# Kernel tuning notes

Hardware: AMD Instinct MI355X
Metric: run time of the kernel (lower is better)

Reference implementation:

```python
import jax, jax.numpy as jnp
import numpy as np
import math

H, NH, LAT = 2048, 16, 512
D = H // NH  # head_dim = 128
B, S = 2, 2048


def setup_inputs() -> dict:
    key = jax.random.key(0)
    ks = jax.random.split(key, 18)
    w = lambda k, i, o: jax.random.normal(k, (i, o), dtype=jnp.float32) * 0.02
    inp = {
        'hidden_states': jax.random.normal(ks[0], (B, S, H), dtype=jnp.float32),
        'attention_mask': jnp.ones((B, S), dtype=jnp.int32),
        'W_DKV': w(ks[1], H, LAT), 'b_DKV': jnp.zeros((LAT,), jnp.float32),
        'W_DQ': w(ks[2], H, LAT), 'b_DQ': jnp.zeros((LAT,), jnp.float32),
        'W_UK': w(ks[3], LAT, H), 'b_UK': jnp.zeros((H,), jnp.float32),
        'W_UV': w(ks[4], LAT, H), 'b_UV': jnp.zeros((H,), jnp.float32),
        'W_UQ': w(ks[5], LAT, H), 'b_UQ': jnp.zeros((H,), jnp.float32),
        'W_KR': w(ks[6], H, D), 'b_KR': jnp.zeros((D,), jnp.float32),
        'W_QR': w(ks[7], H, D), 'b_QR': jnp.zeros((D,), jnp.float32),
        'W_O': w(ks[8], H, H), 'b_O': jnp.zeros((H,), jnp.float32),
    }
    return inp


def _rope(x, seq_len):
    # x: [B, S, D]; rotate-half RoPE exactly as the torch module
    half = D // 2
    inv_freq = 1.0 / (10000.0 ** (jnp.arange(0, D, 2, dtype=jnp.float32) / D))
    ang = jnp.arange(seq_len, dtype=jnp.float32)[:, None] * inv_freq[None, :]  # [S, half]
    sin, cos = jnp.sin(ang), jnp.cos(ang)
    x1, x2 = x[..., :half], x[..., half:]
    return jnp.concatenate([x1 * cos - x2 * sin, x1 * sin + x2 * cos], axis=-1)


def reference(hidden_states, attention_mask, W_DKV, b_DKV, W_DQ, b_DQ,
              W_UK, b_UK, W_UV, b_UV, W_UQ, b_UQ,
              W_KR, b_KR, W_QR, b_QR, W_O, b_O):
    b, s, _ = hidden_states.shape
    c_kv = hidden_states @ W_DKV + b_DKV          # [B,S,LAT]
    c_q = hidden_states @ W_DQ + b_DQ
    k_c = (c_kv @ W_UK + b_UK).reshape(b, s, NH, D).transpose(0, 2, 1, 3)  # [B,H,S,D]
    v_c = (c_kv @ W_UV + b_UV).reshape(b, s, NH, D).transpose(0, 2, 1, 3)
    q_c = (c_q @ W_UQ + b_UQ).reshape(b, s, NH, D).transpose(0, 2, 1, 3)
    k_r = _rope(hidden_states @ W_KR + b_KR, s)[:, None]  # [B,1,S,D] shared across heads
    q_r = _rope(hidden_states @ W_QR + b_QR, s)[:, None]
    scale = 1.0 / math.sqrt(D)
    # q·k with concatenated [compressed | rope] head layout, decomposed to avoid materializing cat
    scores = (jnp.einsum('bhqd,bhkd->bhqk', q_c, k_c)
              + jnp.einsum('bhqd,bhkd->bhqk', q_r, k_r)) * scale  # [B,H,S,S]
    mask = attention_mask[:, None, None, :]
    scores = jnp.where(mask == 0, -jnp.inf, scores)
    attn = jax.nn.softmax(scores, axis=-1)
    ctx = jnp.einsum('bhqk,bhkd->bhqd', attn, v_c)
    ctx = ctx.transpose(0, 2, 1, 3).reshape(b, s, H)
    return ctx @ W_O + b_O
```

## Files before the change

kernel.cpp:

```cpp
#include <hip/hip_runtime.h>
#include <hip/hip_bf16.h>
#include <stdint.h>

typedef __hip_bfloat16 bf16;
typedef __attribute__((ext_vector_type(8))) short s8v;
typedef __attribute__((ext_vector_type(4))) float f4v;

__device__ __forceinline__ void gld16(const bf16* g, bf16* l) {
  __builtin_amdgcn_global_load_lds(
      (__attribute__((address_space(1))) unsigned int*)g,
      (__attribute__((address_space(3))) unsigned int*)l, 16, 0, 0);
}

__device__ __forceinline__ f4v mfma16(s8v a, s8v b, f4v c) {
  return __builtin_amdgcn_mfma_f32_16x16x32_bf16(a, b, c, 0, 0, 0);
}

__device__ __forceinline__ unsigned short f2bfu(float f) {
  union { bf16 h; unsigned short u; } cv;
  cv.h = __float2bfloat16(f);
  return cv.u;
}

__global__ __launch_bounds__(256) void prep(
    const float* __restrict__ hs, bf16* __restrict__ hsb,
    const float* __restrict__ bdkv, const float* __restrict__ bdq,
    const float* __restrict__ bkr, const float* __restrict__ bqr,
    float* __restrict__ bcat,
    const float* __restrict__ wdkv, bf16* __restrict__ tdkv,
    const float* __restrict__ wdq,  bf16* __restrict__ tdq,
    const float* __restrict__ wkr,  bf16* __restrict__ tkr,
    const float* __restrict__ wqr,  bf16* __restrict__ tqr,
    const float* __restrict__ wuk,  bf16* __restrict__ tuk,
    const float* __restrict__ wuv,  bf16* __restrict__ tuv,
    const float* __restrict__ wuq,  bf16* __restrict__ tuq,
    const float* __restrict__ wo,   bf16* __restrict__ to_) {
  int bid = blockIdx.x;
  int tid = threadIdx.x;
  if (bid < 4096) {
    int i = (bid * 256 + tid) * 8;
    union { s8v v; unsigned short u[8]; } pk;
#pragma unroll
    for (int j = 0; j < 8; j++) pk.u[j] = f2bfu(hs[i + j]);
    *(s8v*)(hsb + i) = pk.v;
    return;
  }
  if (bid == 4096) {
#pragma unroll
    for (int p = 0; p < 5; p++) {
      int i = tid + p * 256;
      float v;
      if (i < 512)       v = bdkv[i];
      else if (i < 1024) v = bdq[i - 512];
      else if (i < 1152) v = bkr[i - 1024];
      else               v = bqr[i - 1152];
      bcat[i] = v;
    }
    return;
  }
  bid -= 4097;
  const float* src; bf16* dst; int R, C;
  if      (bid < 1024) { src = wdkv; dst = tdkv; R = 2048; C = 512;  }
  else if (bid < 2048) { src = wdq;  dst = tdq;  R = 2048; C = 512;  bid -= 1024; }
  else if (bid < 2304) { src = wkr;  dst = tkr;  R = 2048; C = 128;  bid -= 2048; }
  else if (bid < 2560) { src = wqr;  dst = tqr;  R = 2048; C = 128;  bid -= 2304; }
  else if (bid < 3584) { src = wuk;  dst = tuk;  R = 512;  C = 2048; bid -= 2560; }
  else if (bid < 4608) { src = wuv;  dst = tuv;  R = 512;  C = 2048; bid -= 3584; }
  else if (bid < 5632) { src = wuq;  dst = tuq;  R = 512;  C = 2048; bid -= 4608; }
  else                 { src = wo;   dst = to_;  R = 2048; C = 2048; bid -= 5632; }
  __shared__ float t[32][33];
  int C32 = C >> 5;
  int bx = bid % C32, by = bid / C32;
  int tx = tid & 31, ty = tid >> 5;
  int c0 = bx * 32, r0 = by * 32;
#pragma unroll
  for (int i = 0; i < 32; i += 8)
    t[ty + i][tx] = src[(size_t)(r0 + ty + i) * C + c0 + tx];
  __syncthreads();
#pragma unroll
  for (int i = 0; i < 32; i += 8)
    dst[(size_t)(c0 + ty + i) * R + r0 + tx] = __float2bfloat16(t[tx][ty + i]);
}

__global__ void rope_kernel(const bf16* __restrict__ inK, bf16* __restrict__ outK,
                            const bf16* __restrict__ inQ, bf16* __restrict__ outQ) {
  const bf16* in = (blockIdx.y == 0) ? inK : inQ;
  bf16* out = (blockIdx.y == 0) ? outK : outQ;
  int row = blockIdx.x;
  int d = threadIdx.x;
  int pos = row & 2047;
  float x1 = __bfloat162float(in[(size_t)row * 128 + d]);
  float x2 = __bfloat162float(in[(size_t)row * 128 + 64 + d]);
  float inv = exp2f(-(float)d * (13.287712379549449f / 64.0f));
  float ang = (float)pos * inv;
  float sn = sinf(ang), cs = cosf(ang);
  out[(size_t)row * 128 + d]      = __float2bfloat16(x1 * cs - x2 * sn);
  out[(size_t)row * 128 + 64 + d] = __float2bfloat16(x1 * sn + x2 * cs);
}

template <int MODE>
__global__ __launch_bounds__(256) void gemm_bt(
    const bf16* __restrict__ A, const bf16* __restrict__ A2,
    const bf16* __restrict__ Bt,
    const float* __restrict__ b0, const float* __restrict__ b1,
    const float* __restrict__ b2,
    void* __restrict__ C0, void* __restrict__ C1,
    void* __restrict__ C2, void* __restrict__ C3,
    int M, int N, int K) {
  __shared__ bf16 sA[128 * 32];
  __shared__ bf16 sB[128 * 32];
  const int tid = threadIdx.x, lane = tid & 63, wid = tid >> 6;
  const int l15 = lane & 15, l4 = lane >> 4;
  const int m0 = blockIdx.y * 128, n0 = blockIdx.x * 128;
  const int wm = (wid >> 1) * 64, wn = (wid & 1) * 64;
  f4v acc[4][4] = {};
  const bf16* Ause = (MODE == 2 && n0 >= 4096) ? A2 : A;
  const bf16* gA = Ause + (size_t)m0 * K;
  const bf16* gB = Bt + (size_t)n0 * K;
  const int row = tid >> 2, col = (tid & 3) * 8;
  for (int k0 = 0; k0 < K; k0 += 32) {
    gld16(gA + (size_t)row * K + k0 + col,        sA + tid * 8);
    gld16(gA + (size_t)(row + 64) * K + k0 + col, sA + (tid + 256) * 8);
    gld16(gB + (size_t)row * K + k0 + col,        sB + tid * 8);
    gld16(gB + (size_t)(row + 64) * K + k0 + col, sB + (tid + 256) * 8);
    __syncthreads();
    s8v a[4], b[4];
#pragma unroll
    for (int i = 0; i < 4; i++) a[i] = *(const s8v*)(sA + (wm + i * 16 + l15) * 32 + l4 * 8);
#pragma unroll
    for (int j = 0; j < 4; j++) b[j] = *(const s8v*)(sB + (wn + j * 16 + l15) * 32 + l4 * 8);
#pragma unroll
    for (int i = 0; i < 4; i++)
#pragma unroll
      for (int j = 0; j < 4; j++) acc[i][j] = mfma16(a[i], b[j], acc[i][j]);
    __syncthreads();
  }
#pragma unroll
  for (int j = 0; j < 4; j++) {
    const int nb = n0 + wn + j * 16;
    const int n = nb + l15;
    if (MODE == 3) {
      const float bv = b0[n];
#pragma unroll
      for (int i = 0; i < 4; i++) {
        size_t mb = m0 + wm + i * 16 + l4 * 4;
#pragma unroll
        for (int g = 0; g < 4; g++)
          ((float*)C0)[(mb + g) * (size_t)N + n] = acc[i][j][g] + bv;
      }
    } else if (MODE == 1) {
      const float bv = b0[n];
      bf16* dst; int stride, nc;
      if (nb < 512)       { dst = (bf16*)C0; stride = 512; nc = n; }
      else if (nb < 1024) { dst = (bf16*)C1; stride = 512; nc = n - 512; }
      else if (nb < 1152) { dst = (bf16*)C2; stride = 128; nc = n - 1024; }
      else                { dst = (bf16*)C3; stride = 128; nc = n - 1152; }
#pragma unroll
      for (int i = 0; i < 4; i++) {
        size_t mb = m0 + wm + i * 16 + l4 * 4;
#pragma unroll
        for (int g = 0; g < 4; g++)
          dst[(mb + g) * (size_t)stride + nc] = __float2bfloat16(acc[i][j][g] + bv);
      }
    } else {
      if (nb < 2048) {
        const float bv = b0[n];
        bf16* dst = (bf16*)C0;
#pragma unroll
        for (int i = 0; i < 4; i++) {
          size_t mb = m0 + wm + i * 16 + l4 * 4;
#pragma unroll
          for (int g = 0; g < 4; g++)
            dst[(mb + g) * (size_t)2048 + n] = __float2bfloat16(acc[i][j][g] + bv);
        }
      } else if (nb < 4096) {
        const float bv = b1[n - 2048];
        bf16* dst = (bf16*)C1;
        int nn = n - 2048, hh = nn >> 7, dd = nn & 127;
#pragma unroll
        for (int i = 0; i < 4; i++) {
          int m = m0 + wm + i * 16 + l4 * 4;
          int bb = m >> 11, ss = m & 2047;
          unsigned int lo = f2bfu(acc[i][j][0] + bv) | ((unsigned int)f2bfu(acc[i][j][1] + bv) << 16);
          unsigned int hi = f2bfu(acc[i][j][2] + bv) | ((unsigned int)f2bfu(acc[i][j][3] + bv) << 16);
          size_t dstoff = ((size_t)(bb * 16 + hh) * 128 + dd) * 2048 + ss;
          uint2 pk; pk.x = lo; pk.y = hi;
          *reinterpret_cast<uint2*>(dst + dstoff) = pk;
        }
      } else {
        const float bv = b2[n - 4096];
        bf16* dst = (bf16*)C2;
        int nn = n - 4096;
#pragma unroll
        for (int i = 0; i < 4; i++) {
          size_t mb = m0 + wm + i * 16 + l4 * 4;
#pragma unroll
          for (int g = 0; g < 4; g++)
            dst[(mb + g) * (size_t)2048 + nn] = __float2bfloat16(acc[i][j][g] + bv);
        }
      }
    }
  }
}

__global__ __launch_bounds__(256, 2) void flash_attn(
    const bf16* __restrict__ Qc, const bf16* __restrict__ Kc,
    const bf16* __restrict__ Qr, const bf16* __restrict__ Kr,
    const bf16* __restrict__ VT, const int* __restrict__ amask,
    bf16* __restrict__ ctx) {
  const int S = 2048, H = 2048, D = 128;
  __shared__ bf16 sK[2][16 * 32 * 8];
  __shared__ bf16 sKr[2][16 * 32 * 8];
  __shared__ bf16 sVT[2][4 * 128 * 8];
  __shared__ bf16 sP[4][4 * 32 * 8];

  const int tid = threadIdx.x, lane = tid & 63, wid = tid >> 6;
  const int l15 = lane & 15, l4 = lane >> 4;
  const int qt = blockIdx.x, bh = blockIdx.y;
  const int b = bh >> 4, h = bh & 15;
  const size_t bS = (size_t)b * S;
  const int q0 = qt * 128 + wid * 32;

  const int keyi = tid & 31, dchi = tid >> 5;
  const int di = tid & 127, kchi = tid >> 7;

  s8v qcf[2][4], qrf[2][4];
#pragma unroll
  for (int r = 0; r < 2; r++) {
    size_t qrow = bS + q0 + r * 16 + l15;
    const bf16* pc = Qc + qrow * H + h * D + l4 * 8;
    const bf16* pr = Qr + qrow * D + l4 * 8;
#pragma unroll
    for (int t = 0; t < 4; t++) {
      qcf[r][t] = *(const s8v*)(pc + t * 32);
      qrf[r][t] = *(const s8v*)(pr + t * 32);
    }
  }

  f4v oacc[2][8] = {};
  float lsum[2][4] = {};
  const float scl = 0.08838834764831845f;

  auto stage = [&](int buf, int kv) {
#pragma unroll
    for (int p = 0; p < 2; p++) {
      int idx = tid + p * 256;
      int key = (idx & 31), dch = (idx >> 5);
      gld16(Kc + (bS + kv + key) * H + h * D + dch * 8, sK[buf] + idx * 8);
      gld16(Kr + (bS + kv + key) * D + dch * 8, sKr[buf] + idx * 8);
      int d = (idx & 127), kch = (idx >> 7);
      gld16(VT + ((size_t)bh * D + d) * S + kv + kch * 8, sVT[buf] + idx * 8);
    }
  };

  stage(0, 0);
  for (int it = 0; it < 64; ++it) {
    const int cur = it & 1;
    __syncthreads();
    if (it + 1 < 64) stage(cur ^ 1, (it + 1) * 32);
    const int kv0 = it * 32;

    int mv[2];
#pragma unroll
    for (int c = 0; c < 2; c++) mv[c] = amask[bS + kv0 + c * 16 + l15];

    f4v sc[2][2] = {};
#pragma unroll
    for (int c = 0; c < 2; c++) {
#pragma unroll
      for (int t = 0; t < 4; t++) {
        s8v kf = *(const s8v*)(sK[cur] + ((t * 4 + l4) * 32 + c * 16 + l15) * 8);
        sc[0][c] = mfma16(qcf[0][t], kf, sc[0][c]);
        sc[1][c] = mfma16(qcf[1][t], kf, sc[1][c]);
      }
#pragma unroll
      for (int t = 0; t < 4; t++) {
        s8v kf = *(const s8v*)(sKr[cur] + ((t * 4 + l4) * 32 + c * 16 + l15) * 8);
        sc[0][c] = mfma16(qrf[0][t], kf, sc[0][c]);
        sc[1][c] = mfma16(qrf[1][t], kf, sc[1][c]);
      }
    }

#pragma unroll
    for (int r = 0; r < 2; r++) {
#pragma unroll
      for (int g = 0; g < 4; g++) {
        int qr_ = r * 16 + l4 * 4 + g;
#pragma unroll
        for (int c = 0; c < 2; c++) {
          float p = (mv[c] == 0) ? 0.f : __expf(sc[r][c][g] * scl);
          lsum[r][g] += p;
          int kch = 2 * c + (l15 >> 3);
          sP[wid][(kch * 32 + qr_) * 8 + (l15 & 7)] = __float2bfloat16(p);
        }
      }
    }
    asm volatile("s_waitcnt lgkmcnt(0)" ::: "memory");

    {
      s8v pf0 = *(const s8v*)(sP[wid] + (l4 * 32 + 0 + l15) * 8);
      s8v pf1 = *(const s8v*)(sP[wid] + (l4 * 32 + 16 + l15) * 8);
#pragma unroll
      for (int c = 0; c < 8; c++) {
        s8v vf = *(const s8v*)(sVT[cur] + (l4 * 128 + c * 16 + l15) * 8);
        oacc[0][c] = mfma16(pf0, vf, oacc[0][c]);
        oacc[1][c] = mfma16(pf1, vf, oacc[1][c]);
      }
    }
  }

#pragma unroll
  for (int r = 0; r < 2; r++)
#pragma unroll
    for (int g = 0; g < 4; g++) {
      float s = lsum[r][g];
#pragma unroll
      for (int off = 8; off; off >>= 1) s += __shfl_xor(s, off, 64);
      lsum[r][g] = 1.0f / s;
    }

#pragma unroll
  for (int r = 0; r < 2; r++) {
#pragma unroll
    for (int c = 0; c < 8; c++) {
#pragma unroll
      for (int g = 0; g < 4; g++) {
        int qrow = q0 + r * 16 + l4 * 4 + g;
        float val = oacc[r][c][g] * lsum[r][g];
        ctx[(bS + qrow) * H + h * D + c * 16 + l15] = __float2bfloat16(val);
      }
    }
  }
}

extern "C" void kernel_launch(void* const* d_in, const int* in_sizes, int n_in,
                              void* d_out, int out_size, void* d_ws, size_t ws_size,
                              hipStream_t stream) {
  const float* hs    = (const float*)d_in[0];
  const int*   amask = (const int*)d_in[1];
  const float* W_DKV = (const float*)d_in[2];  const float* b_DKV = (const float*)d_in[3];
  const float* W_DQ  = (const float*)d_in[4];  const float* b_DQ  = (const float*)d_in[5];
  const float* W_UK  = (const float*)d_in[6];  const float* b_UK  = (const float*)d_in[7];
  const float* W_UV  = (const float*)d_in[8];  const float* b_UV  = (const float*)d_in[9];
  const float* W_UQ  = (const float*)d_in[10]; const float* b_UQ  = (const float*)d_in[11];
  const float* W_KR  = (const float*)d_in[12]; const float* b_KR  = (const float*)d_in[13];
  const float* W_QR  = (const float*)d_in[14]; const float* b_QR  = (const float*)d_in[15];
  const float* W_O   = (const float*)d_in[16]; const float* b_O   = (const float*)d_in[17];

  char* wsb = (char*)d_ws;
  size_t off = 0;
  auto allocB = [&](size_t bytes) {
    void* p = wsb + off; off = (off + bytes + 255) & ~(size_t)255; return p;
  };
  float* bcat  = (float*)allocB(1280 * 4);
  bf16* hsb    = (bf16*)allocB((size_t)4096 * 2048 * 2);
  bf16* wt_dkv = (bf16*)allocB((size_t)512 * 2048 * 2);
  bf16* wt_dq  = (bf16*)allocB((size_t)512 * 2048 * 2);
  bf16* wt_kr  = (bf16*)allocB((size_t)128 * 2048 * 2);
  bf16* wt_qr  = (bf16*)allocB((size_t)128 * 2048 * 2);
  bf16* wt_uk  = (bf16*)allocB((size_t)2048 * 512 * 2);
  bf16* wt_uv  = (bf16*)allocB((size_t)2048 * 512 * 2);
  bf16* wt_uq  = (bf16*)allocB((size_t)2048 * 512 * 2);
  bf16* wt_o   = (bf16*)allocB((size_t)2048 * 2048 * 2);
  bf16* c_kv   = (bf16*)allocB((size_t)4096 * 512 * 2);
  bf16* c_q    = (bf16*)allocB((size_t)4096 * 512 * 2);
  bf16* krl    = (bf16*)allocB((size_t)4096 * 128 * 2);
  bf16* qrl    = (bf16*)allocB((size_t)4096 * 128 * 2);
  bf16* k_r    = (bf16*)allocB((size_t)4096 * 128 * 2);
  bf16* q_r    = (bf16*)allocB((size_t)4096 * 128 * 2);
  bf16* k_c    = (bf16*)allocB((size_t)4096 * 2048 * 2);
  bf16* q_c    = (bf16*)allocB((size_t)4096 * 2048 * 2);
  bf16* vT     = (bf16*)allocB((size_t)4096 * 2048 * 2);
  bf16* ctx    = (bf16*)allocB((size_t)4096 * 2048 * 2);
  (void)wt_uv; (void)wt_uq;

  prep<<<13825, 256, 0, stream>>>(hs, hsb,
      b_DKV, b_DQ, b_KR, b_QR, bcat,
      W_DKV, wt_dkv, W_DQ, wt_dq, W_KR, wt_kr, W_QR, wt_qr,
      W_UK, wt_uk, W_UV, wt_uv, W_UQ, wt_uq, W_O, wt_o);

  gemm_bt<1><<<dim3(10, 32), 256, 0, stream>>>(
      hsb, nullptr, wt_dkv, bcat, nullptr, nullptr,
      c_kv, c_q, krl, qrl, 4096, 1280, 2048);
  rope_kernel<<<dim3(4096, 2), 64, 0, stream>>>(krl, k_r, qrl, q_r);

  gemm_bt<2><<<dim3(48, 32), 256, 0, stream>>>(
      c_kv, c_q, wt_uk, b_UK, b_UV, b_UQ,
      k_c, vT, q_c, nullptr, 4096, 6144, 512);

  flash_attn<<<dim3(16, 32), 256, 0, stream>>>(q_c, k_c, q_r, k_r, vT, amask, ctx);

  gemm_bt<3><<<dim3(16, 32), 256, 0, stream>>>(
      ctx, nullptr, wt_o, b_O, nullptr, nullptr,
      d_out, nullptr, nullptr, nullptr, 4096, 2048, 2048);
}
```

Baseline: 467.0 us.

## Halve flash-attn query tile, load rope keys from global, swizzle P, raise occupancy

The flash attention kernel now handles 16 query rows per wave instead of 32, which doubles the grid and lets four blocks share a CU. Rope key fragments are read straight from global memory (they are shared across heads, so likely cached) rather than staged through LDS. The P buffer gets an XOR swizzle to cut bank conflicts, and s_setprio is raised around the MFMA blocks. In exchange, each K/V tile is reused across half as many queries, so K/V staging traffic per FLOP doubles, and every wave issues its own global rope loads.

```diff
diff --git a/kernel.cpp b/kernel.cpp
--- a/kernel.cpp
+++ b/kernel.cpp
@@ -20,6 +20,10 @@
   union { bf16 h; unsigned short u; } cv;
   cv.h = __float2bfloat16(f);
   return cv.u;
+}
+
+__device__ __forceinline__ int pswz(int rw) {
+  return (rw << 3) ^ (((rw >> 3) & 1) << 4) ^ (((rw >> 4) & 1) << 3);
 }
 
 __global__ __launch_bounds__(256) void prep(
@@ -203,42 +207,37 @@
   }
 }
 
-__global__ __launch_bounds__(256, 2) void flash_attn(
+__global__ __launch_bounds__(256, 4) void flash_attn(
     const bf16* __restrict__ Qc, const bf16* __restrict__ Kc,
     const bf16* __restrict__ Qr, const bf16* __restrict__ Kr,
     const bf16* __restrict__ VT, const int* __restrict__ amask,
     bf16* __restrict__ ctx) {
   const int S = 2048, H = 2048, D = 128;
   __shared__ bf16 sK[2][16 * 32 * 8];
-  __shared__ bf16 sKr[2][16 * 32 * 8];
   __shared__ bf16 sVT[2][4 * 128 * 8];
-  __shared__ bf16 sP[4][4 * 32 * 8];
+  __shared__ bf16 sP[4][4 * 16 * 8];
 
   const int tid = threadIdx.x, lane = tid & 63, wid = tid >> 6;
   const int l15 = lane & 15, l4 = lane >> 4;
   const int qt = blockIdx.x, bh = blockIdx.y;
   const int b = bh >> 4, h = bh & 15;
   const size_t bS = (size_t)b * S;
-  const int q0 = qt * 128 + wid * 32;
-
-  const int keyi = tid & 31, dchi = tid >> 5;
-  const int di = tid & 127, kchi = tid >> 7;
-
-  s8v qcf[2][4], qrf[2][4];
-#pragma unroll
-  for (int r = 0; r < 2; r++) {
-    size_t qrow = bS + q0 + r * 16 + l15;
+  const int q0 = qt * 64 + wid * 16;
+
+  s8v qcf[4], qrf[4];
+  {
+    size_t qrow = bS + q0 + l15;
     const bf16* pc = Qc + qrow * H + h * D + l4 * 8;
     const bf16* pr = Qr + qrow * D + l4 * 8;
 #pragma unroll
     for (int t = 0; t < 4; t++) {
-      qcf[r][t] = *(const s8v*)(pc + t * 32);
-      qrf[r][t] = *(const s8v*)(pr + t * 32);
-    }
-  }
-
-  f4v oacc[2][8] = {};
-  float lsum[2][4] = {};
+      qcf[t] = *(const s8v*)(pc + t * 32);
+      qrf[t] = *(const s8v*)(pr + t * 32);
+    }
+  }
+
+  f4v oacc[8] = {};
+  float lsum[4] = {};
   const float scl = 0.08838834764831845f;
 
   auto stage = [&](int buf, int kv) {
@@ -247,7 +246,6 @@
       int idx = tid + p * 256;
       int key = (idx & 31), dch = (idx >> 5);
       gld16(Kc + (bS + kv + key) * H + h * D + dch * 8, sK[buf] + idx * 8);
-      gld16(Kr + (bS + kv + key) * D + dch * 8, sKr[buf] + idx * 8);
       int d = (idx & 127), kch = (idx >> 7);
       gld16(VT + ((size_t)bh * D + d) * S + kv + kch * 8, sVT[buf] + idx * 8);
     }
@@ -256,79 +254,78 @@
   stage(0, 0);
   for (int it = 0; it < 64; ++it) {
     const int cur = it & 1;
+    const int kv0 = it * 32;
     __syncthreads();
+
+    s8v krf[2][4];
+#pragma unroll
+    for (int c = 0; c < 2; c++)
+#pragma unroll
+      for (int t = 0; t < 4; t++)
+        krf[c][t] = *(const s8v*)(Kr + (bS + kv0 + c * 16 + l15) * (size_t)D + (t * 4 + l4) * 8);
+
     if (it + 1 < 64) stage(cur ^ 1, (it + 1) * 32);
-    const int kv0 = it * 32;
 
     int mv[2];
 #pragma unroll
     for (int c = 0; c < 2; c++) mv[c] = amask[bS + kv0 + c * 16 + l15];
 
-    f4v sc[2][2] = {};
-#pragma unroll
-    for (int c = 0; c < 2; c++) {
+    f4v sc[2] = {};
+    __builtin_amdgcn_s_setprio(1);
+#pragma unroll
+    for (int c = 0; c < 2; c++)
 #pragma unroll
       for (int t = 0; t < 4; t++) {
         s8v kf = *(const s8v*)(sK[cur] + ((t * 4 + l4) * 32 + c * 16 + l15) * 8);
-        sc[0][c] = mfma16(qcf[0][t], kf, sc[0][c]);
-        sc[1][c] = mfma16(qcf[1][t], kf, sc[1][c]);
-      }
-#pragma unroll
-      for (int t = 0; t < 4; t++) {
-        s8v kf = *(const s8v*)(sKr[cur] + ((t * 4 + l4) * 32 + c * 16 + l15) * 8);
-        sc[0][c] = mfma16(qrf[0][t], kf, sc[0][c]);
-        sc[1][c] = mfma16(qrf[1][t], kf, sc[1][c]);
-      }
-    }
-
-#pragma unroll
-    for (int r = 0; r < 2; r++) {
-#pragma unroll
-      for (int g = 0; g < 4; g++) {
-        int qr_ = r * 16 + l4 * 4 + g;
-#pragma unroll
-        for (int c = 0; c < 2; c++) {
-          float p = (mv[c] == 0) ? 0.f : __expf(sc[r][c][g] * scl);
-          lsum[r][g] += p;
-          int kch = 2 * c + (l15 >> 3);
-          sP[wid][(kch * 32 + qr_) * 8 + (l15 & 7)] = __float2bfloat16(p);
-        }
+        sc[c] = mfma16(qcf[t], kf, sc[c]);
+      }
+#pragma unroll
+    for (int c = 0; c < 2; c++)
+#pragma unroll
+      for (int t = 0; t < 4; t++)
+        sc[c] = mfma16(qrf[t], krf[c][t], sc[c]);
+    __builtin_amdgcn_s_setprio(0);
+
+#pragma unroll
+    for (int g = 0; g < 4; g++) {
+      int qr_ = l4 * 4 + g;
+#pragma unroll
+      for (int c = 0; c < 2; c++) {
+        float p = (mv[c] == 0) ? 0.f : __expf(sc[c][g] * scl);
+        lsum[g] += p;
+        int kch = 2 * c + (l15 >> 3);
+        sP[wid][pswz(kch * 16 + qr_) + (l15 & 7)] = __float2bfloat16(p);
       }
     }
     asm volatile("s_waitcnt lgkmcnt(0)" ::: "memory");
 
     {
-      s8v pf0 = *(const s8v*)(sP[wid] + (l4 * 32 + 0 + l15) * 8);
-      s8v pf1 = *(const s8v*)(sP[wid] + (l4 * 32 + 16 + l15) * 8);
+      s8v pf = *(const s8v*)(sP[wid] + pswz(l4 * 16 + l15));
+      __builtin_amdgcn_s_setprio(1);
 #pragma unroll
       for (int c = 0; c < 8; c++) {
         s8v vf = *(const s8v*)(sVT[cur] + (l4 * 128 + c * 16 + l15) * 8);
-        oacc[0][c] = mfma16(pf0, vf, oacc[0][c]);
-        oacc[1][c] = mfma16(pf1, vf, oacc[1][c]);
-      }
-    }
-  }
-
-#pragma unroll
-  for (int r = 0; r < 2; r++)
+        oacc[c] = mfma16(pf, vf, oacc[c]);
+      }
+      __builtin_amdgcn_s_setprio(0);
+    }
+  }
+
+#pragma unroll
+  for (int g = 0; g < 4; g++) {
+    float s = lsum[g];
+#pragma unroll
+    for (int off = 8; off; off >>= 1) s += __shfl_xor(s, off, 64);
+    lsum[g] = 1.0f / s;
+  }
+
+#pragma unroll
+  for (int c = 0; c < 8; c++) {
 #pragma unroll
     for (int g = 0; g < 4; g++) {
-      float s = lsum[r][g];
-#pragma unroll
-      for (int off = 8; off; off >>= 1) s += __shfl_xor(s, off, 64);
-      lsum[r][g] = 1.0f / s;
-    }
-
-#pragma unroll
-  for (int r = 0; r < 2; r++) {
-#pragma unroll
-    for (int c = 0; c < 8; c++) {
-#pragma unroll
-      for (int g = 0; g < 4; g++) {
-        int qrow = q0 + r * 16 + l4 * 4 + g;
-        float val = oacc[r][c][g] * lsum[r][g];
-        ctx[(bS + qrow) * H + h * D + c * 16 + l15] = __float2bfloat16(val);
-      }
+      int qrow = q0 + l4 * 4 + g;
+      float val = oacc[c][g] * lsum[g];
+      ctx[(bS + qrow) * H + h * D + c * 16 + l15] = __float2bfloat16(val);
     }
   }
 }
@@ -388,7 +385,7 @@
       c_kv, c_q, wt_uk, b_UK, b_UV, b_UQ,
       k_c, vT, q_c, nullptr, 4096, 6144, 512);
 
-  flash_attn<<<dim3(16, 32), 256, 0, stream>>>(q_c, k_c, q_r, k_r, vT, amask, ctx);
+  flash_attn<<<dim3(32, 32), 256, 0, stream>>>(q_c, k_c, q_r, k_r, vT, amask, ctx);
 
   gemm_bt<3><<<dim3(16, 32), 256, 0, stream>>>(
       ctx, nullptr, wt_o, b_O, nullptr, nullptr,
```

Result: slower. 818.1 us (+75.2%).

## Compute transposed scores and pass P via ds_bpermute instead of LDS

Applied to the files above, without the earlier changes.

Swaps the QK^T MFMA operands so each lane holds scores for one query across four keys. The probabilities can then be packed into bf16 pairs and redistributed with ds_bpermute into the PV A-operand layout, which removes the per-wave sP shared-memory round trip and its waitcnt. It also loads the attention mask as int4 vectors, keeps one row sum per lane that is reduced with shuffles at the end, and raises wave priority around the MFMA blocks. The cost is extra permute instructions and selects, and more complex lane-mapping logic that could be wrong.

```diff
diff --git a/kernel.cpp b/kernel.cpp
--- a/kernel.cpp
+++ b/kernel.cpp
@@ -212,7 +212,6 @@
   __shared__ bf16 sK[2][16 * 32 * 8];
   __shared__ bf16 sKr[2][16 * 32 * 8];
   __shared__ bf16 sVT[2][4 * 128 * 8];
-  __shared__ bf16 sP[4][4 * 32 * 8];
 
   const int tid = threadIdx.x, lane = tid & 63, wid = tid >> 6;
   const int l15 = lane & 15, l4 = lane >> 4;
@@ -221,9 +220,6 @@
   const size_t bS = (size_t)b * S;
   const int q0 = qt * 128 + wid * 32;
 
-  const int keyi = tid & 31, dchi = tid >> 5;
-  const int di = tid & 127, kchi = tid >> 7;
-
   s8v qcf[2][4], qrf[2][4];
 #pragma unroll
   for (int r = 0; r < 2; r++) {
@@ -238,7 +234,7 @@
   }
 
   f4v oacc[2][8] = {};
-  float lsum[2][4] = {};
+  float lsum[2] = {};
   const float scl = 0.08838834764831845f;
 
   auto stage = [&](int buf, int kv) {
@@ -253,71 +249,94 @@
     }
   };
 
+  const int ae = ((2 * (l4 & 1)) * 16 + l15) * 4;
+  const int ao = ae + 64;
+  const bool mhi = (l4 >= 2);
+
   stage(0, 0);
   for (int it = 0; it < 64; ++it) {
     const int cur = it & 1;
+    const int kv0 = it * 32;
     __syncthreads();
     if (it + 1 < 64) stage(cur ^ 1, (it + 1) * 32);
-    const int kv0 = it * 32;
-
-    int mv[2];
-#pragma unroll
-    for (int c = 0; c < 2; c++) mv[c] = amask[bS + kv0 + c * 16 + l15];
+
+    int4 mv[2];
+#pragma unroll
+    for (int m = 0; m < 2; m++)
+      mv[m] = *(const int4*)(amask + bS + kv0 + m * 16 + l4 * 4);
 
     f4v sc[2][2] = {};
-#pragma unroll
-    for (int c = 0; c < 2; c++) {
+    __builtin_amdgcn_s_setprio(1);
+#pragma unroll
+    for (int m = 0; m < 2; m++)
 #pragma unroll
       for (int t = 0; t < 4; t++) {
-        s8v kf = *(const s8v*)(sK[cur] + ((t * 4 + l4) * 32 + c * 16 + l15) * 8);
-        sc[0][c] = mfma16(qcf[0][t], kf, sc[0][c]);
-        sc[1][c] = mfma16(qcf[1][t], kf, sc[1][c]);
-      }
+        s8v kf = *(const s8v*)(sK[cur] + ((t * 4 + l4) * 32 + m * 16 + l15) * 8);
+        sc[m][0] = mfma16(kf, qcf[0][t], sc[m][0]);
+        sc[m][1] = mfma16(kf, qcf[1][t], sc[m][1]);
+      }
+#pragma unroll
+    for (int m = 0; m < 2; m++)
 #pragma unroll
       for (int t = 0; t < 4; t++) {
-        s8v kf = *(const s8v*)(sKr[cur] + ((t * 4 + l4) * 32 + c * 16 + l15) * 8);
-        sc[0][c] = mfma16(qrf[0][t], kf, sc[0][c]);
-        sc[1][c] = mfma16(qrf[1][t], kf, sc[1][c]);
-      }
-    }
-
+        s8v kf = *(const s8v*)(sKr[cur] + ((t * 4 + l4) * 32 + m * 16 + l15) * 8);
+        sc[m][0] = mfma16(kf, qrf[0][t], sc[m][0]);
+        sc[m][1] = mfma16(kf, qrf[1][t], sc[m][1]);
+      }
+    __builtin_amdgcn_s_setprio(0);
+
+    unsigned int pk[2][2][2];
+#pragma unroll
+    for (int m = 0; m < 2; m++)
+#pragma unroll
+      for (int r = 0; r < 2; r++) {
+        float p0 = mv[m].x ? __expf(sc[m][r][0] * scl) : 0.f;
+        float p1 = mv[m].y ? __expf(sc[m][r][1] * scl) : 0.f;
+        float p2 = mv[m].z ? __expf(sc[m][r][2] * scl) : 0.f;
+        float p3 = mv[m].w ? __expf(sc[m][r][3] * scl) : 0.f;
+        lsum[r] += (p0 + p1) + (p2 + p3);
+        pk[r][m][0] = (unsigned int)f2bfu(p0) | ((unsigned int)f2bfu(p1) << 16);
+        pk[r][m][1] = (unsigned int)f2bfu(p2) | ((unsigned int)f2bfu(p3) << 16);
+      }
+
+    s8v pf[2];
 #pragma unroll
     for (int r = 0; r < 2; r++) {
-#pragma unroll
-      for (int g = 0; g < 4; g++) {
-        int qr_ = r * 16 + l4 * 4 + g;
-#pragma unroll
-        for (int c = 0; c < 2; c++) {
-          float p = (mv[c] == 0) ? 0.f : __expf(sc[r][c][g] * scl);
-          lsum[r][g] += p;
-          int kch = 2 * c + (l15 >> 3);
-          sP[wid][(kch * 32 + qr_) * 8 + (l15 & 7)] = __float2bfloat16(p);
-        }
-      }
-    }
-    asm volatile("s_waitcnt lgkmcnt(0)" ::: "memory");
-
-    {
-      s8v pf0 = *(const s8v*)(sP[wid] + (l4 * 32 + 0 + l15) * 8);
-      s8v pf1 = *(const s8v*)(sP[wid] + (l4 * 32 + 16 + l15) * 8);
-#pragma unroll
-      for (int c = 0; c < 8; c++) {
-        s8v vf = *(const s8v*)(sVT[cur] + (l4 * 128 + c * 16 + l15) * 8);
-        oacc[0][c] = mfma16(pf0, vf, oacc[0][c]);
-        oacc[1][c] = mfma16(pf1, vf, oacc[1][c]);
-      }
-    }
-  }
-
-#pragma unroll
-  for (int r = 0; r < 2; r++)
-#pragma unroll
-    for (int g = 0; g < 4; g++) {
-      float s = lsum[r][g];
-#pragma unroll
-      for (int off = 8; off; off >>= 1) s += __shfl_xor(s, off, 64);
-      lsum[r][g] = 1.0f / s;
-    }
+      int a0 = __builtin_amdgcn_ds_bpermute(ae, (int)pk[r][0][0]);
+      int b0 = __builtin_amdgcn_ds_bpermute(ae, (int)pk[r][1][0]);
+      int a1 = __builtin_amdgcn_ds_bpermute(ae, (int)pk[r][0][1]);
+      int b1 = __builtin_amdgcn_ds_bpermute(ae, (int)pk[r][1][1]);
+      int a2 = __builtin_amdgcn_ds_bpermute(ao, (int)pk[r][0][0]);
+      int b2 = __builtin_amdgcn_ds_bpermute(ao, (int)pk[r][1][0]);
+      int a3 = __builtin_amdgcn_ds_bpermute(ao, (int)pk[r][0][1]);
+      int b3 = __builtin_amdgcn_ds_bpermute(ao, (int)pk[r][1][1]);
+      union { int w[4]; s8v v; } u;
+      u.w[0] = mhi ? b0 : a0;
+      u.w[1] = mhi ? b1 : a1;
+      u.w[2] = mhi ? b2 : a2;
+      u.w[3] = mhi ? b3 : a3;
+      pf[r] = u.v;
+    }
+
+    __builtin_amdgcn_s_setprio(1);
+#pragma unroll
+    for (int c = 0; c < 8; c++) {
+      s8v vf = *(const s8v*)(sVT[cur] + (l4 * 128 + c * 16 + l15) * 8);
+      oacc[0][c] = mfma16(pf[0], vf, oacc[0][c]);
+      oacc[1][c] = mfma16(pf[1], vf, oacc[1][c]);
+    }
+    __builtin_amdgcn_s_setprio(0);
+  }
+
+  float inv[2][4];
+#pragma unroll
+  for (int r = 0; r < 2; r++) {
+    float s = lsum[r];
+    s += __shfl_xor(s, 16, 64);
+    s += __shfl_xor(s, 32, 64);
+#pragma unroll
+    for (int g = 0; g < 4; g++) inv[r][g] = 1.0f / __shfl(s, l4 * 4 + g, 64);
+  }
 
 #pragma unroll
   for (int r = 0; r < 2; r++) {
@@ -326,7 +345,7 @@
 #pragma unroll
       for (int g = 0; g < 4; g++) {
         int qrow = q0 + r * 16 + l4 * 4 + g;
-        float val = oacc[r][c][g] * lsum[r][g];
+        float val = oacc[r][c][g] * inv[r][g];
         ctx[(bS + qrow) * H + h * D + c * 16 + l15] = __float2bfloat16(val);
       }
     }
```

After: 454.2 us. 2.8% less time.
